# Kernel optimization log

Hardware: AMD Instinct MI355X
Metric: run time of the kernel (lower is better)

## Reference

```python
import jax, jax.numpy as jnp
import numpy as np
import math

N_HEAD = 16
EPS = 1e-6


def _phi(x, omega):
    # x: (B, nh, T, d), omega: (d, m) -> (B, nh, T, m)
    m = omega.shape[1]
    proj = jnp.einsum('bhtd,dm->bhtm', x, omega)
    norm_sq_half = 0.5 * jnp.sum(x * x, axis=-1, keepdims=True)
    return jnp.exp(proj - norm_sq_half) / math.sqrt(m)


def setup_inputs() -> dict:
    key = jax.random.key(0)
    ks = jax.random.split(key, 4)
    B, T, C = 2, 1024, 1024
    d_h, m = C // N_HEAD, 128
    x = jax.random.normal(ks[0], (B, T, C), dtype=jnp.float32)
    W_attn = jax.random.normal(ks[1], (C, 3 * C), dtype=jnp.float32) * (1.0 / math.sqrt(C))
    b_attn = jnp.zeros((3 * C,), dtype=jnp.float32)
    W_proj = jax.random.normal(ks[2], (C, C), dtype=jnp.float32) * (1.0 / math.sqrt(C))
    b_proj = jnp.zeros((C,), dtype=jnp.float32)
    omega = jax.random.normal(ks[3], (d_h, m), dtype=jnp.float32)
    return {"x": x, "W_attn": W_attn, "b_attn": b_attn, "W_proj": W_proj, "b_proj": b_proj, "omega": omega}


def reference(x, W_attn, b_attn, W_proj, b_proj, omega):
    B, T, C = x.shape
    nh = N_HEAD
    d_h = C // nh
    # fused QKV projection
    qkv = x @ W_attn + b_attn  # (B, T, 3C)
    q, k, v = jnp.split(qkv, 3, axis=-1)
    # (B, nh, T, d_h)
    q = q.reshape(B, T, nh, d_h).transpose(0, 2, 1, 3)
    k = k.reshape(B, T, nh, d_h).transpose(0, 2, 1, 3)
    v = v.reshape(B, T, nh, d_h).transpose(0, 2, 1, 3)
    scale = 1.0 / math.sqrt(d_h)
    q = q * scale
    k = k * scale
    phi_q = _phi(q, omega)  # (B, nh, T, m)
    phi_k = _phi(k, omega)  # (B, nh, T, m)
    # outer-product state: kv (B, nh, T, m, d_h), causal prefix sums
    kv = phi_k[..., :, None] * v[..., None, :]
    S = jnp.cumsum(kv, axis=2)          # (B, nh, T, m, d_h)
    Z = jnp.cumsum(phi_k, axis=2)       # (B, nh, T, m)
    num = jnp.einsum('bhtm,bhtmd->bhtd', phi_q, S)
    den = jnp.einsum('bhtm,bhtm->bht', phi_q, Z)[..., None] + EPS
    y = num / den                       # (B, nh, T, d_h)
    y = y.transpose(0, 2, 1, 3).reshape(B, T, C)
    return y @ W_proj + b_proj
```

## Files before the change

kernel.cpp:

```cpp
#include <hip/hip_runtime.h>
#include <math.h>

#define B_ 2
#define T_ 1024
#define C_ 1024
#define NH 16
#define DH 64
#define M_ 128
#define LCH 64
#define NC (T_/LCH)
#define DEXT 80

constexpr float SCALE = 0.125f;
constexpr float EPSV = 1e-6f;
constexpr float LOG2E = 1.4426950408889634f;
constexpr float NSQC = -0.72134752044448170f;

typedef _Float16 f16;
typedef f16 f16x4 __attribute__((ext_vector_type(4)));
typedef f16 f16x8 __attribute__((ext_vector_type(8)));
typedef float f32x4 __attribute__((ext_vector_type(4)));

typedef const __attribute__((address_space(1))) void* as1_cvoid_p;
typedef __attribute__((address_space(3))) void* as3_void_p;

#define MFMA16 __builtin_amdgcn_mfma_f32_16x16x32_f16

__device__ __forceinline__ void gload16(const void* g, void* l) {
  __builtin_amdgcn_global_load_lds((as1_cvoid_p)g, (as3_void_p)l, 16, 0, 0);
}

__device__ __forceinline__ float exp2_fast(float x) {
  float r; asm("v_exp_f32 %0, %1" : "=v"(r) : "v"(x)); return r;
}

__device__ __forceinline__ int sw8(int row, int slot)  { return row * 64  + ((slot ^ (row & 7))  << 3); }
__device__ __forceinline__ int sw16(int row, int slot) { return row * 128 + ((slot ^ (row & 15)) << 3); }

__global__ __launch_bounds__(256) void prep_kernel(const float* __restrict__ x,
                                                   const float* __restrict__ omega,
                                                   const float* __restrict__ Wa,
                                                   const float* __restrict__ Wp,
                                                   f16* __restrict__ x16,
                                                   f16* __restrict__ omT,
                                                   f16* __restrict__ vT,
                                                   f16* __restrict__ B16,
                                                   f16* __restrict__ B16p) {
  __shared__ float tile[32][33];
  int bid = blockIdx.x, tid = threadIdx.x;
  if (bid < 2048) {
    int i = (bid * 256 + tid) * 4;
    float4 v = *(const float4*)&x[i];
    f16x4 o = {(f16)v.x, (f16)v.y, (f16)v.z, (f16)v.w};
    *(f16x4*)&x16[i] = o;
  } else if (bid < 2080) {
    int e = (bid - 2048) * 256 + tid;
    int d = e >> 7, m = e & 127;
    omT[m * 64 + d] = (f16)(omega[e] * LOG2E);
  } else if (bid < 2592) {
    int idx = bid - 2080;
    int bh = idx >> 4, dr = idx & 15;
    f16 val = (dr == 0) ? (f16)1.0f : (f16)0.0f;
    f16x4 o = {val, val, val, val};
    *(f16x4*)&vT[((size_t)bh * DEXT + 64 + dr) * 1024 + tid * 4] = o;
  } else {
    int tb = bid - 2592;
    const float* in; f16* out; int N, n0, k0;
    if (tb < 3072) { in = Wa; out = B16;  N = 3072; n0 = (tb % 96) * 32; k0 = (tb / 96) * 32; }
    else { tb -= 3072; in = Wp; out = B16p; N = 1024; n0 = (tb & 31) * 32; k0 = (tb >> 5) * 32; }
    int tx = tid & 31, ty = tid >> 5;
    for (int r = ty; r < 32; r += 8)
      tile[r][tx] = in[(size_t)(k0 + r) * N + n0 + tx];
    __syncthreads();
    for (int r = ty; r < 32; r += 8)
      out[(size_t)(n0 + r) * 1024 + k0 + tx] = (f16)tile[tx][r];
  }
}

__global__ __launch_bounds__(256) void gemm_qkv_kernel(
    const f16* __restrict__ A, const f16* __restrict__ B,
    const float* __restrict__ bias, f16* __restrict__ qk16, f16* __restrict__ vT16) {
  __shared__ f16 As[2][128 * 64];
  __shared__ f16 Bs[2][64 * 64];
  const int tid = threadIdx.x;
  const int wid = tid >> 6, lane = tid & 63;
  const int bm = blockIdx.y * 128, bn = blockIdx.x * 64;
  const int wr = (wid >> 1) * 64, wc = (wid & 1) * 32;
  const int srow = lane >> 3, slot = lane & 7;
  const int frow = lane & 15, fkc = lane >> 4;
  f32x4 acc[4][2];
#pragma unroll
  for (int mi = 0; mi < 4; ++mi)
#pragma unroll
    for (int ni = 0; ni < 2; ++ni) acc[mi][ni] = f32x4{0.f, 0.f, 0.f, 0.f};

  auto STAGE = [&](int buf, int kt) {
#pragma unroll
    for (int i = 0; i < 4; ++i) {
      int row = i * 32 + wid * 8 + srow;
      gload16(&A[(size_t)(bm + row) * 1024 + kt + ((slot ^ (row & 7)) << 3)],
              (char*)As[buf] + i * 4096 + wid * 1024);
    }
#pragma unroll
    for (int i = 0; i < 2; ++i) {
      int row = i * 32 + wid * 8 + srow;
      gload16(&B[(size_t)(bn + row) * 1024 + kt + ((slot ^ (row & 7)) << 3)],
              (char*)Bs[buf] + i * 4096 + wid * 1024);
    }
  };
  STAGE(0, 0);
  for (int kt = 0; kt < 1024; kt += 64) {
    const int cur = (kt >> 6) & 1;
    if (kt + 64 < 1024) {
      STAGE(cur ^ 1, kt + 64);
      asm volatile("s_waitcnt vmcnt(6)" ::: "memory");
    } else {
      asm volatile("s_waitcnt vmcnt(0)" ::: "memory");
    }
    __builtin_amdgcn_s_barrier();
    asm volatile("" ::: "memory");
    f16x8 af[4][2], bf[2][2];
#pragma unroll
    for (int mi = 0; mi < 4; ++mi)
#pragma unroll
      for (int kk = 0; kk < 2; ++kk)
        af[mi][kk] = *(const f16x8*)&As[cur][sw8(wr + mi * 16 + frow, kk * 4 + fkc)];
#pragma unroll
    for (int ni = 0; ni < 2; ++ni)
#pragma unroll
      for (int kk = 0; kk < 2; ++kk)
        bf[ni][kk] = *(const f16x8*)&Bs[cur][sw8(wc + ni * 16 + frow, kk * 4 + fkc)];
#pragma unroll
    for (int kk = 0; kk < 2; ++kk)
#pragma unroll
      for (int mi = 0; mi < 4; ++mi)
#pragma unroll
        for (int ni = 0; ni < 2; ++ni)
          acc[mi][ni] = MFMA16(af[mi][kk], bf[ni][kk], acc[mi][ni], 0, 0, 0);
    asm volatile("" ::: "memory");
    __builtin_amdgcn_s_barrier();
  }
#pragma unroll
  for (int ni = 0; ni < 2; ++ni) {
    int col = bn + wc + ni * 16 + frow;
    float bv = bias[col];
#pragma unroll
    for (int mi = 0; mi < 4; ++mi) {
      int row0 = bm + wr + mi * 16 + (lane >> 4) * 4;
#pragma unroll
      for (int r = 0; r < 4; ++r) {
        int row = row0 + r;
        if (col < 2048) {
          qk16[(size_t)row * 2048 + col] = (f16)((acc[mi][ni][r] + bv) * SCALE);
        } else {
          int cc = col - 2048, hh = cc >> 6, d = cc & 63;
          int b = row >> 10, t = row & 1023;
          vT16[((size_t)(b * 16 + hh) * DEXT + d) * 1024 + t] = (f16)(acc[mi][ni][r] + bv);
        }
      }
    }
  }
}

__global__ __launch_bounds__(256) void gemm_out_kernel(
    const f16* __restrict__ A, const f16* __restrict__ B,
    const float* __restrict__ bias, float* __restrict__ C) {
  __shared__ f16 As[2][128 * 64];
  __shared__ f16 Bs[2][64 * 64];
  const int tid = threadIdx.x;
  const int wid = tid >> 6, lane = tid & 63;
  const int bm = blockIdx.y * 128, bn = blockIdx.x * 64;
  const int wr = (wid >> 1) * 64, wc = (wid & 1) * 32;
  const int srow = lane >> 3, slot = lane & 7;
  const int frow = lane & 15, fkc = lane >> 4;
  f32x4 acc[4][2];
#pragma unroll
  for (int mi = 0; mi < 4; ++mi)
#pragma unroll
    for (int ni = 0; ni < 2; ++ni) acc[mi][ni] = f32x4{0.f, 0.f, 0.f, 0.f};

  auto STAGE = [&](int buf, int kt) {
#pragma unroll
    for (int i = 0; i < 4; ++i) {
      int row = i * 32 + wid * 8 + srow;
      gload16(&A[(size_t)(bm + row) * 1024 + kt + ((slot ^ (row & 7)) << 3)],
              (char*)As[buf] + i * 4096 + wid * 1024);
    }
#pragma unroll
    for (int i = 0; i < 2; ++i) {
      int row = i * 32 + wid * 8 + srow;
      gload16(&B[(size_t)(bn + row) * 1024 + kt + ((slot ^ (row & 7)) << 3)],
              (char*)Bs[buf] + i * 4096 + wid * 1024);
    }
  };
  STAGE(0, 0);
  for (int kt = 0; kt < 1024; kt += 64) {
    const int cur = (kt >> 6) & 1;
    if (kt + 64 < 1024) {
      STAGE(cur ^ 1, kt + 64);
      asm volatile("s_waitcnt vmcnt(6)" ::: "memory");
    } else {
      asm volatile("s_waitcnt vmcnt(0)" ::: "memory");
    }
    __builtin_amdgcn_s_barrier();
    asm volatile("" ::: "memory");
    f16x8 af[4][2], bf[2][2];
#pragma unroll
    for (int mi = 0; mi < 4; ++mi)
#pragma unroll
      for (int kk = 0; kk < 2; ++kk)
        af[mi][kk] = *(const f16x8*)&As[cur][sw8(wr + mi * 16 + frow, kk * 4 + fkc)];
#pragma unroll
    for (int ni = 0; ni < 2; ++ni)
#pragma unroll
      for (int kk = 0; kk < 2; ++kk)
        bf[ni][kk] = *(const f16x8*)&Bs[cur][sw8(wc + ni * 16 + frow, kk * 4 + fkc)];
#pragma unroll
    for (int kk = 0; kk < 2; ++kk)
#pragma unroll
      for (int mi = 0; mi < 4; ++mi)
#pragma unroll
        for (int ni = 0; ni < 2; ++ni)
          acc[mi][ni] = MFMA16(af[mi][kk], bf[ni][kk], acc[mi][ni], 0, 0, 0);
    asm volatile("" ::: "memory");
    __builtin_amdgcn_s_barrier();
  }
#pragma unroll
  for (int ni = 0; ni < 2; ++ni) {
    int col = bn + wc + ni * 16 + frow;
    float bv = bias[col];
#pragma unroll
    for (int mi = 0; mi < 4; ++mi) {
      int row0 = bm + wr + mi * 16 + (lane >> 4) * 4;
#pragma unroll
      for (int r = 0; r < 4; ++r)
        C[(size_t)(row0 + r) * 1024 + col] = acc[mi][ni][r] + bv;
    }
  }
}

__global__ __launch_bounds__(256) void chunkS_kernel(const f16* __restrict__ qk16,
                                                     const f16* __restrict__ omT,
                                                     const f16* __restrict__ vT,
                                                     f16* __restrict__ ST) {
  __shared__ f16 k_s[4096];
  __shared__ f16 pkT_s[8192];
  __shared__ f16 vt_s[5120];
  __shared__ float nsq_s[64];
  const int tid = threadIdx.x;
  const int wid = tid >> 6, lane = tid & 63;
  const int bc = blockIdx.x;
  const int bh = bc / NC, c = bc % NC;
  const int b = bh >> 4, h = bh & 15;
  const int tbase = c * LCH;
  const int frow = lane & 15, fkc = lane >> 4;
  {
    int rbase = b * 1024 + tbase, cbase = 1024 + h * 64;
#pragma unroll
    for (int r = 0; r < 2; ++r) {
      int row = r * 32 + wid * 8 + (lane >> 3);
      gload16(qk16 + (size_t)(rbase + row) * 2048 + cbase + ((lane & 7) ^ (row & 7)) * 8,
              (char*)k_s + r * 4096 + wid * 1024);
    }
  }
  for (int rr = wid; rr < 10; rr += 4) {
    int d = rr * 8 + (lane >> 3);
    gload16(vT + ((size_t)bh * DEXT + d) * 1024 + tbase + ((lane & 7) ^ (d & 7)) * 8,
            (char*)vt_s + rr * 1024);
  }
  __syncthreads();
  if (tid < 64) {
    float s = 0.f;
#pragma unroll
    for (int j = 0; j < 8; ++j) {
      f16x8 v = *(const f16x8*)&k_s[sw8(tid, j)];
#pragma unroll
      for (int e = 0; e < 8; ++e) { float f = (float)v[e]; s += f * f; }
    }
    nsq_s[tid] = s;
  }
  f32x4 acc2[8];
#pragma unroll
  for (int cm = 0; cm < 8; ++cm) acc2[cm] = f32x4{0.f, 0.f, 0.f, 0.f};
  {
    f16x8 af2[2], bf2;
#pragma unroll
    for (int kk = 0; kk < 2; ++kk)
      af2[kk] = *(const f16x8*)&k_s[sw8(wid * 16 + frow, kk * 4 + fkc)];
#pragma unroll
    for (int cm = 0; cm < 8; ++cm)
#pragma unroll
      for (int kk = 0; kk < 2; ++kk) {
        bf2 = *(const f16x8*)&omT[(cm * 16 + frow) * 64 + kk * 32 + fkc * 8];
        acc2[cm] = MFMA16(af2[kk], bf2, acc2[cm], 0, 0, 0);
      }
  }
  __syncthreads();
  {
    int t0g = wid * 16 + (lane >> 4) * 4;
    int slot = t0g >> 3, sub = t0g & 4;
    float4 n4 = *(float4*)&nsq_s[t0g];
    float nn[4] = {NSQC * n4.x - 3.5f, NSQC * n4.y - 3.5f,
                   NSQC * n4.z - 3.5f, NSQC * n4.w - 3.5f};
#pragma unroll
    for (int cm = 0; cm < 8; ++cm) {
      int m = cm * 16 + frow;
      f16x4 o;
#pragma unroll
      for (int r = 0; r < 4; ++r)
        o[r] = (f16)exp2_fast(acc2[cm][r] + nn[r]);
      *(f16x4*)&pkT_s[m * 64 + ((slot ^ (m & 7)) << 3) + sub] = o;
    }
  }
  __syncthreads();
  f32x4 acc[5][2];
#pragma unroll
  for (int dt = 0; dt < 5; ++dt)
#pragma unroll
    for (int cj = 0; cj < 2; ++cj) acc[dt][cj] = f32x4{0.f, 0.f, 0.f, 0.f};
  f16x8 af, bf[2][2];
#pragma unroll
  for (int cj = 0; cj < 2; ++cj)
#pragma unroll
    for (int kk = 0; kk < 2; ++kk)
      bf[cj][kk] = *(const f16x8*)&pkT_s[sw8(wid * 32 + cj * 16 + frow, kk * 4 + fkc)];
#pragma unroll
  for (int dt = 0; dt < 5; ++dt)
#pragma unroll
    for (int kk = 0; kk < 2; ++kk) {
      af = *(const f16x8*)&vt_s[sw8(dt * 16 + frow, kk * 4 + fkc)];
#pragma unroll
      for (int cj = 0; cj < 2; ++cj)
        acc[dt][cj] = MFMA16(af, bf[cj][kk], acc[dt][cj], 0, 0, 0);
    }
  f16* dst = ST + (size_t)bc * (DEXT * 128);
#pragma unroll
  for (int dt = 0; dt < 5; ++dt)
#pragma unroll
    for (int cj = 0; cj < 2; ++cj) {
      int m = wid * 32 + cj * 16 + frow;
      int d0 = dt * 16 + (lane >> 4) * 4;
#pragma unroll
      for (int r = 0; r < 4; ++r)
        dst[(size_t)(d0 + r) * 128 + m] = (f16)acc[dt][cj][r];
    }
}

__global__ __launch_bounds__(256) void prefix_kernel(f16* __restrict__ ST) {
  int tid = threadIdx.x;
  int bh = blockIdx.x;
  int d = blockIdx.y * 16 + (tid >> 4), m0 = (tid & 15) * 8;
  float run[8] = {};
  for (int c = 0; c < NC; ++c) {
    f16* p = ST + ((size_t)(bh * NC + c) * DEXT + d) * 128 + m0;
    f16x8 v = *(f16x8*)p;
    f16x8 o;
#pragma unroll
    for (int j = 0; j < 8; ++j) {
      o[j] = (f16)run[j];
      run[j] += (float)v[j];
    }
    *(f16x8*)p = o;
  }
}

__global__ __launch_bounds__(256) void intra_kernel(const f16* __restrict__ qk16,
    const f16* __restrict__ omT, const f16* __restrict__ vT,
    const f16* __restrict__ ST, f16* __restrict__ y16) {
  __shared__ f16 pq_s[8192];
  __shared__ f16 pk_s[8192];
  __shared__ f16 vt_s[5120];
  __shared__ f16 st_s[10240];
  __shared__ f16 qk2_s[8192];
  __shared__ float nsq_s[128];
  __shared__ float den_s[64];
  f16* q_s = qk2_s;
  f16* k_s = qk2_s + 4096;
  f16* a_s = qk2_s;
  const int tid = threadIdx.x;
  const int wid = tid >> 6, lane = tid & 63;
  const int bc = blockIdx.x;
  const int bh = bc / NC, c = bc % NC;
  const int b = bh >> 4, h = bh & 15;
  const int tbase = c * LCH;
  const int frow = lane & 15, fkc = lane >> 4;
  {
    int rbase = b * 1024 + tbase;
#pragma unroll
    for (int r = 0; r < 2; ++r) {
      int row = r * 32 + wid * 8 + (lane >> 3);
      int csw = ((lane & 7) ^ (row & 7)) * 8;
      gload16(qk16 + (size_t)(rbase + row) * 2048 + h * 64 + csw,
              (char*)q_s + r * 4096 + wid * 1024);
      gload16(qk16 + (size_t)(rbase + row) * 2048 + 1024 + h * 64 + csw,
              (char*)k_s + r * 4096 + wid * 1024);
    }
  }
  for (int rr = wid; rr < 10; rr += 4) {
    int d = rr * 8 + (lane >> 3);
    gload16(vT + ((size_t)bh * DEXT + d) * 1024 + tbase + ((lane & 7) ^ (d & 7)) * 8,
            (char*)vt_s + rr * 1024);
  }
#pragma unroll
  for (int r = 0; r < 5; ++r) {
    int row = r * 16 + wid * 4 + (lane >> 4);
    int col = ((lane & 15) ^ (row & 15)) * 8;
    gload16(ST + (size_t)bc * (DEXT * 128) + (size_t)row * 128 + col,
            (char*)st_s + r * 4096 + wid * 1024);
  }
  __syncthreads();
  if (tid < 128) {
    const f16* src = (tid < 64) ? q_s : k_s;
    int t = tid & 63;
    float s = 0.f;
#pragma unroll
    for (int j = 0; j < 8; ++j) {
      f16x8 v = *(const f16x8*)&src[sw8(t, j)];
#pragma unroll
      for (int e = 0; e < 8; ++e) { float f = (float)v[e]; s += f * f; }
    }
    nsq_s[tid] = s;
  }
  f32x4 acc1q[2][4], acc1k[2][4];
#pragma unroll
  for (int mi = 0; mi < 2; ++mi)
#pragma unroll
    for (int ct = 0; ct < 4; ++ct) {
      acc1q[mi][ct] = f32x4{0.f, 0.f, 0.f, 0.f};
      acc1k[mi][ct] = f32x4{0.f, 0.f, 0.f, 0.f};
    }
  {
    f16x8 af[2][2], bfq, bfk;
#pragma unroll
    for (int mi = 0; mi < 2; ++mi)
#pragma unroll
      for (int kk = 0; kk < 2; ++kk)
        af[mi][kk] = *(const f16x8*)&omT[(wid * 32 + mi * 16 + frow) * 64 + kk * 32 + fkc * 8];
#pragma unroll
    for (int ct = 0; ct < 4; ++ct)
#pragma unroll
      for (int kk = 0; kk < 2; ++kk) {
        bfq = *(const f16x8*)&q_s[sw8(ct * 16 + frow, kk * 4 + fkc)];
        bfk = *(const f16x8*)&k_s[sw8(ct * 16 + frow, kk * 4 + fkc)];
#pragma unroll
        for (int mi = 0; mi < 2; ++mi) {
          acc1q[mi][ct] = MFMA16(af[mi][kk], bfq, acc1q[mi][ct], 0, 0, 0);
          acc1k[mi][ct] = MFMA16(af[mi][kk], bfk, acc1k[mi][ct], 0, 0, 0);
        }
      }
  }
  __syncthreads();
#pragma unroll
  for (int ct = 0; ct < 4; ++ct) {
    int t = ct * 16 + frow;
    float nq = NSQC * nsq_s[t] - 3.5f, nk = NSQC * nsq_s[64 + t] - 3.5f;
#pragma unroll
    for (int mi = 0; mi < 2; ++mi) {
      int m0 = wid * 32 + mi * 16 + (lane >> 4) * 4;
      int addr = t * 128 + (((m0 >> 3) ^ (t & 15)) << 3) + (m0 & 4);
      f16x4 oq, ok;
#pragma unroll
      for (int r = 0; r < 4; ++r) {
        oq[r] = (f16)exp2_fast(acc1q[mi][ct][r] + nq);
        ok[r] = (f16)exp2_fast(acc1k[mi][ct][r] + nk);
      }
      *(f16x4*)&pq_s[addr] = oq;
      *(f16x4*)&pk_s[addr] = ok;
    }
  }
  __syncthreads();
  {
    f32x4 accq[4];
#pragma unroll
    for (int ct = 0; ct < 4; ++ct) accq[ct] = f32x4{0.f, 0.f, 0.f, 0.f};
    f16x8 af[4], bf;
#pragma unroll
    for (int kk = 0; kk < 4; ++kk)
      af[kk] = *(const f16x8*)&pk_s[sw16(wid * 16 + frow, kk * 4 + fkc)];
#pragma unroll
    for (int ct = 0; ct < 4; ++ct)
#pragma unroll
      for (int kk = 0; kk < 4; ++kk) {
        bf = *(const f16x8*)&pq_s[sw16(ct * 16 + frow, kk * 4 + fkc)];
        accq[ct] = MFMA16(af[kk], bf, accq[ct], 0, 0, 0);
      }
    int tkbase = wid * 16 + fkc * 4;
    int slot = tkbase >> 3, sub = tkbase & 4;
#pragma unroll
    for (int ct = 0; ct < 4; ++ct) {
      int tq = ct * 16 + frow;
      f16x4 av;
#pragma unroll
      for (int r = 0; r < 4; ++r)
        av[r] = (f16)((tkbase + r <= tq) ? accq[ct][r] : 0.f);
      *(f16x4*)&a_s[tq * 64 + ((slot ^ (tq & 7)) << 3) + sub] = av;
    }
  }
  __syncthreads();
  f32x4 acc2[5];
#pragma unroll
  for (int ct = 0; ct < 5; ++ct) acc2[ct] = f32x4{0.f, 0.f, 0.f, 0.f};
  {
    f16x8 afA[2], afP[4], bfv;
#pragma unroll
    for (int kk = 0; kk < 2; ++kk)
      afA[kk] = *(const f16x8*)&a_s[sw8(wid * 16 + frow, kk * 4 + fkc)];
#pragma unroll
    for (int kk = 0; kk < 4; ++kk)
      afP[kk] = *(const f16x8*)&pq_s[sw16(wid * 16 + frow, kk * 4 + fkc)];
#pragma unroll
    for (int ct = 0; ct < 5; ++ct) {
#pragma unroll
      for (int kk = 0; kk < 2; ++kk) {
        bfv = *(const f16x8*)&vt_s[sw8(ct * 16 + frow, kk * 4 + fkc)];
        acc2[ct] = MFMA16(afA[kk], bfv, acc2[ct], 0, 0, 0);
      }
#pragma unroll
      for (int kk = 0; kk < 4; ++kk) {
        bfv = *(const f16x8*)&st_s[sw16(ct * 16 + frow, kk * 4 + fkc)];
        acc2[ct] = MFMA16(afP[kk], bfv, acc2[ct], 0, 0, 0);
      }
    }
  }
  if (frow == 0) {
    int t0g = wid * 16 + (lane >> 4) * 4;
#pragma unroll
    for (int r = 0; r < 4; ++r) den_s[t0g + r] = acc2[4][r];
  }
  __syncthreads();
  {
    int t0g = wid * 16 + (lane >> 4) * 4;
    float4 d4 = *(float4*)&den_s[t0g];
    float inv[4] = {1.f / (d4.x + EPSV), 1.f / (d4.y + EPSV),
                    1.f / (d4.z + EPSV), 1.f / (d4.w + EPSV)};
#pragma unroll
    for (int ct = 0; ct < 4; ++ct) {
      int d = ct * 16 + frow;
#pragma unroll
      for (int r = 0; r < 4; ++r) {
        int t = t0g + r;
        y16[(size_t)(b * 1024 + tbase + t) * 1024 + h * 64 + d] =
            (f16)(acc2[ct][r] * inv[r]);
      }
    }
  }
}

extern "C" void kernel_launch(void* const* d_in, const int* in_sizes, int n_in,
                              void* d_out, int out_size, void* d_ws, size_t ws_size,
                              hipStream_t stream) {
  const float* x      = (const float*)d_in[0];
  const float* W_attn = (const float*)d_in[1];
  const float* b_attn = (const float*)d_in[2];
  const float* W_proj = (const float*)d_in[3];
  const float* b_proj = (const float*)d_in[4];
  const float* omega  = (const float*)d_in[5];
  float* out = (float*)d_out;

  char* base = (char*)d_ws;
  f16* x16    = (f16*)(base);
  f16* B16    = (f16*)(base + 4194304);
  f16* qk16   = (f16*)(base + 10485760);
  f16* vT16   = (f16*)(base + 18874368);
  f16* ST     = (f16*)(base + 24117248);
  f16* omT16  = (f16*)(base + 34603008);
  f16* B16p   = (f16*)(base + 34619392);
  f16* y16    = (f16*)(base + 36716544);

  prep_kernel<<<6688, 256, 0, stream>>>(x, omega, W_attn, W_proj, x16, omT16, vT16, B16, B16p);
  gemm_qkv_kernel<<<dim3(48, 16), 256, 0, stream>>>(x16, B16, b_attn, qk16, vT16);
  chunkS_kernel<<<512, 256, 0, stream>>>(qk16, omT16, vT16, ST);
  prefix_kernel<<<dim3(32, 5), 256, 0, stream>>>(ST);
  intra_kernel<<<512, 256, 0, stream>>>(qk16, omT16, vT16, ST, y16);
  gemm_out_kernel<<<dim3(16, 16), 256, 0, stream>>>(y16, B16p, b_proj, out);
}
```

Measured before the change: 73.43 us.

## Synthesize ones/zero vT rows in LDS, stage omega in LDS, overlap ST load

The ones/zero padding rows of vT are now written directly into shared memory inside chunkS and intra kernels instead of being stored to global by prep_kernel and reloaded, which shrinks prep's grid and the global loads. In intra_kernel, omega is staged into swizzled LDS via async loads instead of per-lane global reads. The ST chunk load is issued after the phi computation so it overlaps with the next MFMA stage, with LDS reused through aliasing (st_s over om_s) and an explicit vmcnt wait. Aliasing adds correctness risk around the timing of overwrites.

```diff
diff --git a/kernel.cpp b/kernel.cpp
--- a/kernel.cpp
+++ b/kernel.cpp
@@ -43,7 +43,6 @@
                                                    const float* __restrict__ Wp,
                                                    f16* __restrict__ x16,
                                                    f16* __restrict__ omT,
-                                                   f16* __restrict__ vT,
                                                    f16* __restrict__ B16,
                                                    f16* __restrict__ B16p) {
   __shared__ float tile[32][33];
@@ -57,14 +56,8 @@
     int e = (bid - 2048) * 256 + tid;
     int d = e >> 7, m = e & 127;
     omT[m * 64 + d] = (f16)(omega[e] * LOG2E);
-  } else if (bid < 2592) {
-    int idx = bid - 2080;
-    int bh = idx >> 4, dr = idx & 15;
-    f16 val = (dr == 0) ? (f16)1.0f : (f16)0.0f;
-    f16x4 o = {val, val, val, val};
-    *(f16x4*)&vT[((size_t)bh * DEXT + 64 + dr) * 1024 + tid * 4] = o;
   } else {
-    int tb = bid - 2592;
+    int tb = bid - 2080;
     const float* in; f16* out; int N, n0, k0;
     if (tb < 3072) { in = Wa; out = B16;  N = 3072; n0 = (tb % 96) * 32; k0 = (tb / 96) * 32; }
     else { tb -= 3072; in = Wp; out = B16p; N = 1024; n0 = (tb & 31) * 32; k0 = (tb >> 5) * 32; }
@@ -263,10 +256,16 @@
               (char*)k_s + r * 4096 + wid * 1024);
     }
   }
-  for (int rr = wid; rr < 10; rr += 4) {
+  for (int rr = wid; rr < 8; rr += 4) {
     int d = rr * 8 + (lane >> 3);
     gload16(vT + ((size_t)bh * DEXT + d) * 1024 + tbase + ((lane & 7) ^ (d & 7)) * 8,
             (char*)vt_s + rr * 1024);
+  }
+  {
+    int row = 64 + (tid >> 4), c4 = (tid & 15) * 4;
+    f16 val = (row == 64) ? (f16)1.0f : (f16)0.0f;
+    f16x4 o = {val, val, val, val};
+    *(f16x4*)&vt_s[row * 64 + c4] = o;
   }
   __syncthreads();
   if (tid < 64) {
@@ -370,13 +369,14 @@
   __shared__ f16 pq_s[8192];
   __shared__ f16 pk_s[8192];
   __shared__ f16 vt_s[5120];
-  __shared__ f16 st_s[10240];
-  __shared__ f16 qk2_s[8192];
+  __shared__ f16 r2[16384];
   __shared__ float nsq_s[128];
   __shared__ float den_s[64];
-  f16* q_s = qk2_s;
-  f16* k_s = qk2_s + 4096;
-  f16* a_s = qk2_s;
+  f16* om_s = r2;
+  f16* q_s  = r2 + 8192;
+  f16* k_s  = r2 + 12288;
+  f16* st_s = r2;
+  f16* a_s  = r2 + 10240;
   const int tid = threadIdx.x;
   const int wid = tid >> 6, lane = tid & 63;
   const int bc = blockIdx.x;
@@ -384,6 +384,12 @@
   const int b = bh >> 4, h = bh & 15;
   const int tbase = c * LCH;
   const int frow = lane & 15, fkc = lane >> 4;
+#pragma unroll
+  for (int r = 0; r < 4; ++r) {
+    int row = r * 32 + wid * 8 + (lane >> 3);
+    gload16(omT + row * 64 + ((lane & 7) ^ (row & 7)) * 8,
+            (char*)om_s + r * 4096 + wid * 1024);
+  }
   {
     int rbase = b * 1024 + tbase;
 #pragma unroll
@@ -396,11 +402,78 @@
               (char*)k_s + r * 4096 + wid * 1024);
     }
   }
-  for (int rr = wid; rr < 10; rr += 4) {
+  for (int rr = wid; rr < 8; rr += 4) {
     int d = rr * 8 + (lane >> 3);
     gload16(vT + ((size_t)bh * DEXT + d) * 1024 + tbase + ((lane & 7) ^ (d & 7)) * 8,
             (char*)vt_s + rr * 1024);
   }
+  {
+    int row = 64 + (tid >> 4), c4 = (tid & 15) * 4;
+    f16 val = (row == 64) ? (f16)1.0f : (f16)0.0f;
+    f16x4 o = {val, val, val, val};
+    *(f16x4*)&vt_s[row * 64 + c4] = o;
+  }
+  __syncthreads();
+  if (tid < 128) {
+    const f16* src = (tid < 64) ? q_s : k_s;
+    int t = tid & 63;
+    float s = 0.f;
+#pragma unroll
+    for (int j = 0; j < 8; ++j) {
+      f16x8 v = *(const f16x8*)&src[sw8(t, j)];
+#pragma unroll
+      for (int e = 0; e < 8; ++e) { float f = (float)v[e]; s += f * f; }
+    }
+    nsq_s[tid] = s;
+  }
+  f32x4 acc1q[2][4], acc1k[2][4];
+#pragma unroll
+  for (int mi = 0; mi < 2; ++mi)
+#pragma unroll
+    for (int ct = 0; ct < 4; ++ct) {
+      acc1q[mi][ct] = f32x4{0.f, 0.f, 0.f, 0.f};
+      acc1k[mi][ct] = f32x4{0.f, 0.f, 0.f, 0.f};
+    }
+  {
+    f16x8 af[2][2], bfq, bfk;
+#pragma unroll
+    for (int mi = 0; mi < 2; ++mi)
+#pragma unroll
+      for (int kk = 0; kk < 2; ++kk)
+        af[mi][kk] = *(const f16x8*)&om_s[sw8(wid * 32 + mi * 16 + frow, kk * 4 + fkc)];
+#pragma unroll
+    for (int ct = 0; ct < 4; ++ct)
+#pragma unroll
+      for (int kk = 0; kk < 2; ++kk) {
+        bfq = *(const f16x8*)&q_s[sw8(ct * 16 + frow, kk * 4 + fkc)];
+        bfk = *(const f16x8*)&k_s[sw8(ct * 16 + frow, kk * 4 + fkc)];
+#pragma unroll
+        for (int mi = 0; mi < 2; ++mi) {
+          acc1q[mi][ct] = MFMA16(af[mi][kk], bfq, acc1q[mi][ct], 0, 0, 0);
+          acc1k[mi][ct] = MFMA16(af[mi][kk], bfk, acc1k[mi][ct], 0, 0, 0);
+        }
+      }
+  }
+  __syncthreads();
+#pragma unroll
+  for (int ct = 0; ct < 4; ++ct) {
+    int t = ct * 16 + frow;
+    float nq = NSQC * nsq_s[t] - 3.5f, nk = NSQC * nsq_s[64 + t] - 3.5f;
+#pragma unroll
+    for (int mi = 0; mi < 2; ++mi) {
+      int m0 = wid * 32 + mi * 16 + (lane >> 4) * 4;
+      int addr = t * 128 + (((m0 >> 3) ^ (t & 15)) << 3) + (m0 & 4);
+      f16x4 oq, ok;
+#pragma unroll
+      for (int r = 0; r < 4; ++r) {
+        oq[r] = (f16)exp2_fast(acc1q[mi][ct][r] + nq);
+        ok[r] = (f16)exp2_fast(acc1k[mi][ct][r] + nk);
+      }
+      *(f16x4*)&pq_s[addr] = oq;
+      *(f16x4*)&pk_s[addr] = ok;
+    }
+  }
+  __syncthreads();
 #pragma unroll
   for (int r = 0; r < 5; ++r) {
     int row = r * 16 + wid * 4 + (lane >> 4);
@@ -408,67 +481,6 @@
     gload16(ST + (size_t)bc * (DEXT * 128) + (size_t)row * 128 + col,
             (char*)st_s + r * 4096 + wid * 1024);
   }
-  __syncthreads();
-  if (tid < 128) {
-    const f16* src = (tid < 64) ? q_s : k_s;
-    int t = tid & 63;
-    float s = 0.f;
-#pragma unroll
-    for (int j = 0; j < 8; ++j) {
-      f16x8 v = *(const f16x8*)&src[sw8(t, j)];
-#pragma unroll
-      for (int e = 0; e < 8; ++e) { float f = (float)v[e]; s += f * f; }
-    }
-    nsq_s[tid] = s;
-  }
-  f32x4 acc1q[2][4], acc1k[2][4];
-#pragma unroll
-  for (int mi = 0; mi < 2; ++mi)
-#pragma unroll
-    for (int ct = 0; ct < 4; ++ct) {
-      acc1q[mi][ct] = f32x4{0.f, 0.f, 0.f, 0.f};
-      acc1k[mi][ct] = f32x4{0.f, 0.f, 0.f, 0.f};
-    }
-  {
-    f16x8 af[2][2], bfq, bfk;
-#pragma unroll
-    for (int mi = 0; mi < 2; ++mi)
-#pragma unroll
-      for (int kk = 0; kk < 2; ++kk)
-        af[mi][kk] = *(const f16x8*)&omT[(wid * 32 + mi * 16 + frow) * 64 + kk * 32 + fkc * 8];
-#pragma unroll
-    for (int ct = 0; ct < 4; ++ct)
-#pragma unroll
-      for (int kk = 0; kk < 2; ++kk) {
-        bfq = *(const f16x8*)&q_s[sw8(ct * 16 + frow, kk * 4 + fkc)];
-        bfk = *(const f16x8*)&k_s[sw8(ct * 16 + frow, kk * 4 + fkc)];
-#pragma unroll
-        for (int mi = 0; mi < 2; ++mi) {
-          acc1q[mi][ct] = MFMA16(af[mi][kk], bfq, acc1q[mi][ct], 0, 0, 0);
-          acc1k[mi][ct] = MFMA16(af[mi][kk], bfk, acc1k[mi][ct], 0, 0, 0);
-        }
-      }
-  }
-  __syncthreads();
-#pragma unroll
-  for (int ct = 0; ct < 4; ++ct) {
-    int t = ct * 16 + frow;
-    float nq = NSQC * nsq_s[t] - 3.5f, nk = NSQC * nsq_s[64 + t] - 3.5f;
-#pragma unroll
-    for (int mi = 0; mi < 2; ++mi) {
-      int m0 = wid * 32 + mi * 16 + (lane >> 4) * 4;
-      int addr = t * 128 + (((m0 >> 3) ^ (t & 15)) << 3) + (m0 & 4);
-      f16x4 oq, ok;
-#pragma unroll
-      for (int r = 0; r < 4; ++r) {
-        oq[r] = (f16)exp2_fast(acc1q[mi][ct][r] + nq);
-        ok[r] = (f16)exp2_fast(acc1k[mi][ct][r] + nk);
-      }
-      *(f16x4*)&pq_s[addr] = oq;
-      *(f16x4*)&pk_s[addr] = ok;
-    }
-  }
-  __syncthreads();
   {
     f32x4 accq[4];
 #pragma unroll
@@ -496,6 +508,7 @@
       *(f16x4*)&a_s[tq * 64 + ((slot ^ (tq & 7)) << 3) + sub] = av;
     }
   }
+  asm volatile("s_waitcnt vmcnt(0)" ::: "memory");
   __syncthreads();
   f32x4 acc2[5];
 #pragma unroll
@@ -567,7 +580,7 @@
   f16* B16p   = (f16*)(base + 34619392);
   f16* y16    = (f16*)(base + 36716544);
 
-  prep_kernel<<<6688, 256, 0, stream>>>(x, omega, W_attn, W_proj, x16, omT16, vT16, B16, B16p);
+  prep_kernel<<<6176, 256, 0, stream>>>(x, omega, W_attn, W_proj, x16, omT16, B16, B16p);
   gemm_qkv_kernel<<<dim3(48, 16), 256, 0, stream>>>(x16, B16, b_attn, qk16, vT16);
   chunkS_kernel<<<512, 256, 0, stream>>>(qk16, omT16, vT16, ST);
   prefix_kernel<<<dim3(32, 5), 256, 0, stream>>>(ST);
```

Result: no change. 72.46 us (-1.3%).
